# Kernel tuning notes

Measured on AMD Instinct MI355X. Metric: run time of the kernel, lower is better.

The kernel has to match this reference:

```python
import jax, jax.numpy as jnp
import numpy as np

B, NTH, NTW, M, DF = 64, 56, 56, 8, 8
FAR = 100.0  # sentinel location for off sources, as in the torch module


def setup_inputs() -> dict:
    key = jax.random.key(0)
    k1, k2, k3, k4, k5 = jax.random.split(key, 5)
    est_locs = jax.random.uniform(k1, (B, NTH, NTW, M, 2), dtype=jnp.float32)
    true_locs = jax.random.uniform(k2, (B, NTH, NTW, M, 2), dtype=jnp.float32)
    true_fluxes = jax.random.normal(k3, (B, NTH, NTW, M, DF), dtype=jnp.float32)
    est_n_sources = jax.random.randint(k4, (B, NTH, NTW), 0, M + 1, dtype=jnp.int32)
    true_n_sources = jax.random.randint(k5, (B, NTH, NTW), 0, M + 1, dtype=jnp.int32)
    return {"est_locs": est_locs, "true_locs": true_locs, "true_fluxes": true_fluxes,
            "est_n_sources": est_n_sources, "true_n_sources": true_n_sources}


def reference(est_locs, true_locs, true_fluxes, est_n_sources, true_n_sources):
    b, nth, ntw, m, _ = est_locs.shape
    T = b * nth * ntw
    slot = jnp.arange(m)
    # is_on_mask per tile: first n_sources slots are on
    est_on = slot[None, :] < est_n_sources.reshape(T, 1)    # [T, m] bool
    true_on = slot[None, :] < true_n_sources.reshape(T, 1)  # [T, m] bool

    # masked locs -> pairwise L2 distances (torch.cdist p=2)
    el = jnp.where(est_on[..., None], est_locs.reshape(T, m, 2), jnp.float32(FAR))
    tl = jnp.where(true_on[..., None], true_locs.reshape(T, m, 2), jnp.float32(FAR))
    diff = el[:, :, None, :] - tl[:, None, :, :]
    dist = jnp.sqrt(jnp.sum(diff * diff, axis=-1))  # [T, m, m]

    # _fast_one_to_one_match
    match1 = jnp.argmin(dist, axis=1)  # best est row per true col  [T, m]
    match2 = jnp.argmin(dist, axis=2)  # best true col per est row  [T, m]
    match1cond2 = jnp.take_along_axis(match1, match2, axis=1)
    one2one = match1cond2 == slot[None, :]
    est_out = match1 > (est_on.sum(-1, keepdims=True) - 1)
    true_out = match2 > (true_on.sum(-1, keepdims=True) - 1)
    one2one = one2one & ~(est_out | true_out)
    # unmatched pairs point to the padded dump slot m (== est_to_true*mask + offset)
    est_idx = jnp.where(one2one, match1, m)
    true_idx = jnp.where(one2one, match2, m)

    # flat indices across (b*nth*ntw) tiles, each of width m+1
    tile_off = (jnp.arange(T) * (m + 1))[:, None]
    flat_est = (est_idx + tile_off).reshape(-1)
    flat_true = (true_idx + tile_off).reshape(-1)

    # padded true catalog: locs(2) | fluxes(DF) | n_sources-indicator(1)
    fields = jnp.concatenate([
        true_locs.reshape(T, m, 2),
        true_fluxes.reshape(T, m, -1),
        true_on[..., None].astype(jnp.float32),
    ], axis=-1)  # [T, m, 2+DF+1]
    d = fields.shape[-1]
    padded = jnp.concatenate([fields, jnp.zeros((T, 1, d), fields.dtype)], axis=1)
    padded = padded.reshape(T * (m + 1), d)

    # gather matched true rows, scatter into est positions (zeros init)
    target = jnp.zeros_like(padded).at[flat_est].set(padded[flat_true])
    target = target.reshape(T, m + 1, d)[:, :m]  # drop dump slot (v[..., :-1, :])
    return target.reshape(b, nth, ntw, m, d)
```

## Files before the change

### kernel.cpp

```cpp
#include <hip/hip_runtime.h>
#include <math.h>

constexpr int TT = 64 * 56 * 56;
__global__ __launch_bounds__(64) void mvd_fused_branchless(
    const float4* __restrict__ el4,
    const float4* __restrict__ tl4,
    const float*  __restrict__ tf,
    const int*    __restrict__ en_,
    const int*    __restrict__ tn_,
    float4*       __restrict__ out4)
{
#pragma clang fp contract(off)
    const int lane = threadIdx.x;
    const int t0   = blockIdx.x * 64;
    const int t    = t0 + lane;

    int rowsrc = 0;
    {
        const int en = en_[t];
        const int tn = tn_[t];

        float4 ea = el4[t * 4 + 0], eb = el4[t * 4 + 1];
        float4 ec = el4[t * 4 + 2], ed = el4[t * 4 + 3];
        float4 ta = tl4[t * 4 + 0], tb = tl4[t * 4 + 1];
        float4 tc = tl4[t * 4 + 2], td = tl4[t * 4 + 3];

        float mex[8], mey[8], mtx[8], mty[8];
        {
            const float exs[8] = {ea.x, ea.z, eb.x, eb.z, ec.x, ec.z, ed.x, ed.z};
            const float eys[8] = {ea.y, ea.w, eb.y, eb.w, ec.y, ec.w, ed.y, ed.w};
            const float txs[8] = {ta.x, ta.z, tb.x, tb.z, tc.x, tc.z, td.x, td.z};
            const float tys[8] = {ta.y, ta.w, tb.y, tb.w, tc.y, tc.w, td.y, td.w};
#pragma unroll
            for (int i = 0; i < 8; i++) {
                mex[i] = (i < en) ? exs[i] : 100.0f;
                mey[i] = (i < en) ? eys[i] : 100.0f;
                mtx[i] = (i < tn) ? txs[i] : 100.0f;
                mty[i] = (i < tn) ? tys[i] : 100.0f;
            }
        }

        float colmin[8];
        int   m1[8], m2[8];
#pragma unroll
        for (int j = 0; j < 8; j++) { colmin[j] = 1e30f; m1[j] = 0; }
#pragma unroll
        for (int i = 0; i < 8; i++) {
            float rmin = 1e30f;
            int   rj = 0;
#pragma unroll
            for (int j = 0; j < 8; j++) {
                float dx = mex[i] - mtx[j];
                float dy = mey[i] - mty[j];
                float dx2 = dx * dx;
                float dy2 = dy * dy;
                float d = sqrtf(dx2 + dy2);
                if (d < rmin) { rmin = d; rj = j; }
                if (d < colmin[j]) { colmin[j] = d; m1[j] = i; }
            }
            m2[i] = rj;
        }

        int m1p = 0;
#pragma unroll
        for (int j = 0; j < 8; j++) m1p |= m1[j] << (3 * j);

#pragma unroll
        for (int k = 0; k < 8; k++) {
            int j = m2[k];
            int m1j = (m1p >> (3 * j)) & 7;
            bool o2o = (m1j == k) && (m1[k] < en) && (m2[k] < tn);
            if (o2o) {
                int r = m1[k];
                rowsrc = (rowsrc & ~(0xF << (4 * r))) | ((8 | j) << (4 * r));
            }
        }
    }

    const float* tl = (const float*)tl4;
    float4* oblk = out4 + (size_t)t0 * 22;

#pragma unroll
    for (int it = 0; it < 22; it++) {
        const int i   = lane + it * 64;
        const int tl_ = (i * 2979) >> 16;
        const int q   = i - tl_ * 22;
        const int w   = __shfl(rowsrc, tl_);
        const int tt  = t0 + tl_;

        float res[4];
#pragma unroll
        for (int u = 0; u < 4; u++) {
            const int p = 4 * q + u;
            const int r = (p * 94) >> 10;
            const int c = p - r * 11;
            const int v = (w >> (4 * r)) & 15;
            const int j = v & 7;
            const bool matched = (v & 8) != 0;

            const float* ptl = tl + ((tt << 4) + (j << 1) + (c & 1));
            const float* ptf = tf + ((tt << 6) + (j << 3) + (c - 2));
            const float* pr  = (c < 2) ? ptl : ptf;
            pr = (matched && c < 10) ? pr : (tl + (tt << 4));
            const float val = *pr;

            const float sel = (c == 10) ? 1.0f : val;
            res[u] = matched ? sel : 0.0f;
        }
        oblk[i] = make_float4(res[0], res[1], res[2], res[3]);
    }
}

extern "C" void kernel_launch(void* const* d_in, const int* in_sizes, int n_in,
                              void* d_out, int out_size, void* d_ws, size_t ws_size,
                              hipStream_t stream) {
    const float* est_locs    = (const float*)d_in[0];
    const float* true_locs   = (const float*)d_in[1];
    const float* true_fluxes = (const float*)d_in[2];
    const int*   est_n       = (const int*)d_in[3];
    const int*   true_n      = (const int*)d_in[4];
    float* out = (float*)d_out;

    mvd_fused_branchless<<<TT / 64, 64, 0, stream>>>(
        (const float4*)est_locs, (const float4*)true_locs, true_fluxes,
        est_n, true_n, (float4*)out);
}
```

Before: 150.6 us.

## Map each tile to eight lanes with shuffle-based matching and LDS-staged output

Replaces the one-thread-per-tile kernel with a cooperative scheme in which eight lanes share a tile, one per source slot. Distances are computed per row using shuffles, column argmins come from xor-shuffle reductions plus ballot, and the match word is assembled across lanes. Each lane gathers its matched row with vector loads and writes it into shared memory, and the tile block is then copied out with coalesced float4 stores. This cuts per-thread register pressure and raises parallelism, at the cost of extra shuffles and a block-wide barrier.

After: 128.9 us. 1.17x faster.

```diff
diff --git a/kernel.cpp b/kernel.cpp
--- a/kernel.cpp
+++ b/kernel.cpp
@@ -2,112 +2,111 @@
 #include <math.h>
 
 constexpr int TT = 64 * 56 * 56;
-__global__ __launch_bounds__(64) void mvd_fused_branchless(
-    const float4* __restrict__ el4,
-    const float4* __restrict__ tl4,
-    const float*  __restrict__ tf,
+__global__ __launch_bounds__(256) void mvd_coop(
+    const float2* __restrict__ el2,
+    const float2* __restrict__ tl2,
+    const float4* __restrict__ tf4,
     const int*    __restrict__ en_,
     const int*    __restrict__ tn_,
     float4*       __restrict__ out4)
 {
 #pragma clang fp contract(off)
-    const int lane = threadIdx.x;
-    const int t0   = blockIdx.x * 64;
-    const int t    = t0 + lane;
+    const int w    = threadIdx.x >> 6;
+    const int L    = threadIdx.x & 63;
+    const int tloc = L >> 3;
+    const int r    = L & 7;
+    const int tb   = blockIdx.x * 32 + w * 8;
+    const int gt   = tb + tloc;
+    const int g    = gt * 8 + r;
 
-    int rowsrc = 0;
-    {
-        const int en = en_[t];
-        const int tn = tn_[t];
+    __shared__ float s_buf[4][704];
+    float* sw = s_buf[w];
 
-        float4 ea = el4[t * 4 + 0], eb = el4[t * 4 + 1];
-        float4 ec = el4[t * 4 + 2], ed = el4[t * 4 + 3];
-        float4 ta = tl4[t * 4 + 0], tb = tl4[t * 4 + 1];
-        float4 tc = tl4[t * 4 + 2], td = tl4[t * 4 + 3];
+    const int en = en_[gt];
+    const int tn = tn_[gt];
 
-        float mex[8], mey[8], mtx[8], mty[8];
-        {
-            const float exs[8] = {ea.x, ea.z, eb.x, eb.z, ec.x, ec.z, ed.x, ed.z};
-            const float eys[8] = {ea.y, ea.w, eb.y, eb.w, ec.y, ec.w, ed.y, ed.w};
-            const float txs[8] = {ta.x, ta.z, tb.x, tb.z, tc.x, tc.z, td.x, td.z};
-            const float tys[8] = {ta.y, ta.w, tb.y, tb.w, tc.y, tc.w, td.y, td.w};
+    const float2 eL = el2[g];
+    const float2 tL = tl2[g];
+
+    const float ex = (r < en) ? eL.x : 100.0f;
+    const float ey = (r < en) ? eL.y : 100.0f;
+    const float tx = (r < tn) ? tL.x : 100.0f;
+    const float ty = (r < tn) ? tL.y : 100.0f;
+
+    float d[8];
 #pragma unroll
-            for (int i = 0; i < 8; i++) {
-                mex[i] = (i < en) ? exs[i] : 100.0f;
-                mey[i] = (i < en) ? eys[i] : 100.0f;
-                mtx[i] = (i < tn) ? txs[i] : 100.0f;
-                mty[i] = (i < tn) ? tys[i] : 100.0f;
-            }
-        }
-
-        float colmin[8];
-        int   m1[8], m2[8];
-#pragma unroll
-        for (int j = 0; j < 8; j++) { colmin[j] = 1e30f; m1[j] = 0; }
-#pragma unroll
-        for (int i = 0; i < 8; i++) {
-            float rmin = 1e30f;
-            int   rj = 0;
-#pragma unroll
-            for (int j = 0; j < 8; j++) {
-                float dx = mex[i] - mtx[j];
-                float dy = mey[i] - mty[j];
-                float dx2 = dx * dx;
-                float dy2 = dy * dy;
-                float d = sqrtf(dx2 + dy2);
-                if (d < rmin) { rmin = d; rj = j; }
-                if (d < colmin[j]) { colmin[j] = d; m1[j] = i; }
-            }
-            m2[i] = rj;
-        }
-
-        int m1p = 0;
-#pragma unroll
-        for (int j = 0; j < 8; j++) m1p |= m1[j] << (3 * j);
-
-#pragma unroll
-        for (int k = 0; k < 8; k++) {
-            int j = m2[k];
-            int m1j = (m1p >> (3 * j)) & 7;
-            bool o2o = (m1j == k) && (m1[k] < en) && (m2[k] < tn);
-            if (o2o) {
-                int r = m1[k];
-                rowsrc = (rowsrc & ~(0xF << (4 * r))) | ((8 | j) << (4 * r));
-            }
-        }
+    for (int j = 0; j < 8; j++) {
+        const float txj = __shfl(tx, j, 8);
+        const float tyj = __shfl(ty, j, 8);
+        const float dx = ex - txj;
+        const float dy = ey - tyj;
+        const float dx2 = dx * dx;
+        const float dy2 = dy * dy;
+        d[j] = sqrtf(dx2 + dy2);
     }
 
-    const float* tl = (const float*)tl4;
-    float4* oblk = out4 + (size_t)t0 * 22;
+    float rmin = 1e30f; int m2o = 0;
+#pragma unroll
+    for (int j = 0; j < 8; j++)
+        if (d[j] < rmin) { rmin = d[j]; m2o = j; }
 
+    const int gbase = L & 56;
+    int m1p = 0;
 #pragma unroll
-    for (int it = 0; it < 22; it++) {
-        const int i   = lane + it * 64;
-        const int tl_ = (i * 2979) >> 16;
-        const int q   = i - tl_ * 22;
-        const int w   = __shfl(rowsrc, tl_);
-        const int tt  = t0 + tl_;
+    for (int j = 0; j < 8; j++) {
+        float dm = d[j];
+#pragma unroll
+        for (int s = 1; s < 8; s <<= 1) {
+            const float o = __shfl_xor(dm, s);
+            dm = (o < dm) ? o : dm;
+        }
+        const unsigned long long bal = __ballot(d[j] == dm);
+        const int b = (int)((bal >> gbase) & 0xFFull);
+        m1p |= (__ffs(b) - 1) << (3 * j);
+    }
 
-        float res[4];
+    const int m1r = (m1p >> (3 * r)) & 7;
+    const int m1j = (m1p >> (3 * m2o)) & 7;
+    const bool o2o = (m1j == r) && (m1r < en) && (m2o < tn);
+
+    const int contrib = o2o ? ((8 | m2o) << (4 * m1r)) : 0;
+    const int cmask   = o2o ? (0xF      << (4 * m1r)) : 0;
+    int wrd = 0;
 #pragma unroll
-        for (int u = 0; u < 4; u++) {
-            const int p = 4 * q + u;
-            const int r = (p * 94) >> 10;
-            const int c = p - r * 11;
-            const int v = (w >> (4 * r)) & 15;
-            const int j = v & 7;
-            const bool matched = (v & 8) != 0;
+    for (int s = 0; s < 8; s++) {
+        const int cw = __shfl(contrib, s, 8);
+        const int cm = __shfl(cmask,  s, 8);
+        wrd = (wrd & ~cm) | cw;
+    }
 
-            const float* ptl = tl + ((tt << 4) + (j << 1) + (c & 1));
-            const float* ptf = tf + ((tt << 6) + (j << 3) + (c - 2));
-            const float* pr  = (c < 2) ? ptl : ptf;
-            pr = (matched && c < 10) ? pr : (tl + (tt << 4));
-            const float val = *pr;
+    const int  v = (wrd >> (4 * r)) & 15;
+    const bool matched = (v & 8) != 0;
+    const int  j = v & 7;
 
-            const float sel = (c == 10) ? 1.0f : val;
-            res[u] = matched ? sel : 0.0f;
-        }
-        oblk[i] = make_float4(res[0], res[1], res[2], res[3]);
+    float o0=0,o1=0,o2=0,o3=0,o4=0,o5=0,o6=0,o7=0,o8=0,o9=0,o10=0;
+    if (matched) {
+        const int sr = gt * 8 + j;
+        const float2 p  = tl2[sr];
+        const float4 f0 = tf4[2 * sr];
+        const float4 f1 = tf4[2 * sr + 1];
+        o0 = p.x;  o1 = p.y;
+        o2 = f0.x; o3 = f0.y; o4 = f0.z; o5 = f0.w;
+        o6 = f1.x; o7 = f1.y; o8 = f1.z; o9 = f1.w;
+        o10 = 1.0f;
+    }
+    {
+        float* row = sw + tloc * 88 + r * 11;
+        row[0]=o0; row[1]=o1; row[2]=o2; row[3]=o3; row[4]=o4; row[5]=o5;
+        row[6]=o6; row[7]=o7; row[8]=o8; row[9]=o9; row[10]=o10;
+    }
+    __syncthreads();
+
+    const float4* sw4 = (const float4*)sw;
+    float4* ob = out4 + (size_t)tb * 22;
+#pragma unroll
+    for (int k = 0; k < 3; k++) {
+        const int fidx = L + 64 * k;
+        if (fidx < 176) ob[fidx] = sw4[fidx];
     }
 }
 
@@ -121,7 +120,7 @@
     const int*   true_n      = (const int*)d_in[4];
     float* out = (float*)d_out;
 
-    mvd_fused_branchless<<<TT / 64, 64, 0, stream>>>(
-        (const float4*)est_locs, (const float4*)true_locs, true_fluxes,
-        est_n, true_n, (float4*)out);
+    mvd_coop<<<TT / 32, 256, 0, stream>>>(
+        (const float2*)est_locs, (const float2*)true_locs,
+        (const float4*)true_fluxes, est_n, true_n, (float4*)out);
 }
```
